# Optimization experiments

Hardware: AMD Instinct MI355X
Metric: run time of the kernel (lower is better)

## Reference

```python
import jax, jax.numpy as jnp
import numpy as np

SIGMA = 5.0
KSIZE = 31  # int(6*sigma+1), odd
CHANNEL = 3

def build_gaussian_kernel(size, sigma):
    coords = jnp.arange(size, dtype=jnp.float32) - size // 2
    g = jnp.exp(-coords ** 2 / (2.0 * sigma ** 2))
    g = g / g.sum()
    k2d = g[:, None] * g[None, :]            # (k, k)
    # depthwise kernel: (O=C, I/g=1, k, k)
    return jnp.broadcast_to(k2d[None, None], (CHANNEL, 1, size, size))

def depthwise_blur(x, kernel):
    # x: (B, C, H, W); kernel: (C, 1, k, k); groups = C, SAME-style padding k//2
    pad = KSIZE // 2
    return jax.lax.conv_general_dilated(
        x, kernel,
        window_strides=(1, 1),
        padding=((pad, pad), (pad, pad)),
        dimension_numbers=("NCHW", "OIHW", "NCHW"),
        feature_group_count=CHANNEL,
    )

def setup_inputs() -> dict:
    key = jax.random.key(0)
    k1, k2 = jax.random.split(key)
    B, C, H, W = 16, 3, 512, 512
    background = jax.random.uniform(k1, (B, C, H, W), dtype=jnp.float32)
    insatance = jax.random.uniform(k2, (B, C, H, W), dtype=jnp.float32)
    gaussian_kernel = build_gaussian_kernel(KSIZE, SIGMA)
    return {"background": background, "insatance": insatance,
            "gaussian_kernel": gaussian_kernel}

def reference(background, insatance, gaussian_kernel):
    # retinex_decompose(background): only illumination1 is used downstream
    bg_log = jnp.log1p(background)
    illumination1 = depthwise_blur(bg_log, gaussian_kernel)
    # retinex_decompose(insatance): reflectance2 = log1p(ins) - blur(log1p(ins))
    ins_log = jnp.log1p(insatance)
    illumination2 = depthwise_blur(ins_log, gaussian_kernel)
    reflectance2 = ins_log - illumination2
    # adjust_illumination(reflectance2, illumination1)
    img_log = reflectance2 + illumination1
    img_corrected = jnp.clip(jnp.expm1(img_log), 0.0, 1.0)
    return img_corrected
```

## Files before the change

### kernel.cpp

```cpp
#include <hip/hip_runtime.h>


constexpr int W_ = 512, H_ = 512;
constexpr int NIMG = 48;
constexpr int TW = 64, TH = 64;
constexpr int R_ = TH + 30;
constexpr int CSLOT = 24;
constexpr int DSTRIDE = 25;
constexpr int HSTRIDE = 17;

__device__ constexpr float G[31] = {
    8.8805851e-04f, 1.5861066e-03f, 2.7217699e-03f, 4.4874399e-03f,
    7.1084368e-03f, 1.0818767e-02f, 1.5820117e-02f, 2.2226435e-02f,
    3.0002549e-02f, 3.8911209e-02f, 4.8486352e-02f, 5.8048702e-02f,
    6.6771901e-02f, 7.3794364e-02f, 7.8357552e-02f, 7.9940480e-02f,
    7.8357552e-02f, 7.3794364e-02f, 6.6771901e-02f, 5.8048702e-02f,
    4.8486352e-02f, 3.8911209e-02f, 3.0002549e-02f, 2.2226435e-02f,
    1.5820117e-02f, 1.0818767e-02f, 7.1084368e-03f, 4.4874399e-03f,
    2.7217699e-03f, 1.5861066e-03f, 8.8805851e-04f};

__global__ __launch_bounds__(256) void retinex_fused(const float* __restrict__ bg,
                                                     const float* __restrict__ ins,
                                                     float* __restrict__ out) {
  __shared__ float4 sd[R_ * DSTRIDE];
  __shared__ float4 sh[R_ * HSTRIDE];

  const int tid = threadIdx.x;
  const int x0 = blockIdx.x * TW;
  const int y0 = blockIdx.y * TH;
  const size_t base = (size_t)blockIdx.z * ((size_t)H_ * W_);

#pragma unroll
  for (int it = 0; it < 9; ++it) {
    const int idx = tid + 256 * it;
    if (idx < R_ * CSLOT) {
      const int r = idx / CSLOT;
      const int c = idx - r * CSLOT;
      const int y = y0 - 15 + r;
      const int gx = x0 - 16 + 4 * c;
      float4 v = make_float4(0.f, 0.f, 0.f, 0.f);
      if ((unsigned)y < (unsigned)H_ && (unsigned)gx < (unsigned)W_) {
        const size_t a = base + (size_t)y * W_ + gx;
        const float4 b = *(const float4*)(bg + a);
        const float4 n = *(const float4*)(ins + a);
        v.x = __logf(1.f + b.x) - __logf(1.f + n.x);
        v.y = __logf(1.f + b.y) - __logf(1.f + n.y);
        v.z = __logf(1.f + b.z) - __logf(1.f + n.z);
        v.w = __logf(1.f + b.w) - __logf(1.f + n.w);
      }
      sd[r * DSTRIDE + c] = v;
    }
  }
  __syncthreads();

#pragma unroll
  for (int it = 0; it < 3; ++it) {
    const int idx = tid + 256 * it;
    if (idx < R_ * 8) {
      const int r = idx >> 3;
      const int w = idx & 7;
      float win[40];
      const float4* p = &sd[r * DSTRIDE + 2 * w];
#pragma unroll
      for (int k = 0; k < 10; ++k) {
        const float4 v = p[k];
        win[4 * k + 0] = v.x; win[4 * k + 1] = v.y;
        win[4 * k + 2] = v.z; win[4 * k + 3] = v.w;
      }
      float o[8];
#pragma unroll
      for (int e = 0; e < 8; ++e) {
        float a = 0.f;
#pragma unroll
        for (int c = 0; c < 31; ++c) a += G[c] * win[e + 1 + c];
        o[e] = a;
      }
      sh[r * HSTRIDE + 2 * w]     = make_float4(o[0], o[1], o[2], o[3]);
      sh[r * HSTRIDE + 2 * w + 1] = make_float4(o[4], o[5], o[6], o[7]);
    }
  }
  __syncthreads();

  {
    const int col = tid & 63;
    const int g = tid >> 6;
    const float* hf = (const float*)sh;
    float acc[16];
#pragma unroll
    for (int p = 0; p < 16; ++p) acc[p] = 0.f;
#pragma unroll
    for (int j = 0; j < 46; ++j) {
      const float v = hf[(16 * g + j) * (HSTRIDE * 4) + col];
#pragma unroll
      for (int p = 0; p < 16; ++p) {
        const int c = j - p;
        if (c >= 0 && c < 31) acc[p] += G[c] * v;
      }
    }
#pragma unroll
    for (int p = 0; p < 16; ++p) {
      const int y = y0 + 16 * g + p;
      const size_t idx = base + (size_t)y * W_ + x0 + col;
      const float il = __logf(1.f + ins[idx]);
      float r = __expf(il + acc[p]) - 1.f;
      out[idx] = fminf(fmaxf(r, 0.f), 1.f);
    }
  }
}

extern "C" void kernel_launch(void* const* d_in, const int* in_sizes, int n_in,
                              void* d_out, int out_size, void* d_ws, size_t ws_size,
                              hipStream_t stream) {
  const float* bg  = (const float*)d_in[0];
  const float* ins = (const float*)d_in[1];
  float* out = (float*)d_out;
  retinex_fused<<<dim3(W_ / TW, H_ / TH, NIMG), dim3(256), 0, stream>>>(bg, ins, out);
}
```

Baseline: 188.8 us.

## Split blur into vertical and horizontal passes through a transposed workspace

Replaces the single fused kernel with two kernels. The first does the vertical blur on log-differences and writes a transposed intermediate. The second reads that transposed data, so its horizontal blur becomes a column-wise register sweep, then applies the expm1 and clip. This removes the shared-memory horizontal pass and its halo columns, at the cost of an extra global write and read of a full intermediate buffer plus a second launch. If the workspace is too small it writes into an input buffer, which is risky.

```diff
diff --git a/kernel.cpp b/kernel.cpp
--- a/kernel.cpp
+++ b/kernel.cpp
@@ -1,13 +1,10 @@
 #include <hip/hip_runtime.h>
 
 
-constexpr int W_ = 512, H_ = 512;
-constexpr int NIMG = 48;
-constexpr int TW = 64, TH = 64;
-constexpr int R_ = TH + 30;
-constexpr int CSLOT = 24;
-constexpr int DSTRIDE = 25;
-constexpr int HSTRIDE = 17;
+constexpr int W_ = 512, H_ = 512, NIMG = 48;
+constexpr int TS = 64;
+constexpr int RS = 94;
+constexpr int PITCH = 68;
 
 __device__ constexpr float G[31] = {
     8.8805851e-04f, 1.5861066e-03f, 2.7217699e-03f, 4.4874399e-03f,
@@ -19,28 +16,25 @@
     1.5820117e-02f, 1.0818767e-02f, 7.1084368e-03f, 4.4874399e-03f,
     2.7217699e-03f, 1.5861066e-03f, 8.8805851e-04f};
 
-__global__ __launch_bounds__(256) void retinex_fused(const float* __restrict__ bg,
-                                                     const float* __restrict__ ins,
-                                                     float* __restrict__ out) {
-  __shared__ float4 sd[R_ * DSTRIDE];
-  __shared__ float4 sh[R_ * HSTRIDE];
-
-  const int tid = threadIdx.x;
-  const int x0 = blockIdx.x * TW;
-  const int y0 = blockIdx.y * TH;
+__global__ __launch_bounds__(256) void vpass(const float* __restrict__ bg,
+                                             const float* __restrict__ ins,
+                                             float* __restrict__ tmpT) {
+  __shared__ __align__(16) float sb[RS * PITCH];
+  const int tid  = threadIdx.x;
+  const int lane = tid & 63;
+  const int w    = tid >> 6;
+  const int x0 = blockIdx.x * TS, y0 = blockIdx.y * TS;
   const size_t base = (size_t)blockIdx.z * ((size_t)H_ * W_);
 
 #pragma unroll
-  for (int it = 0; it < 9; ++it) {
+  for (int it = 0; it < 6; ++it) {
     const int idx = tid + 256 * it;
-    if (idx < R_ * CSLOT) {
-      const int r = idx / CSLOT;
-      const int c = idx - r * CSLOT;
+    if (idx < RS * 16) {
+      const int r = idx >> 4, c = idx & 15;
       const int y = y0 - 15 + r;
-      const int gx = x0 - 16 + 4 * c;
       float4 v = make_float4(0.f, 0.f, 0.f, 0.f);
-      if ((unsigned)y < (unsigned)H_ && (unsigned)gx < (unsigned)W_) {
-        const size_t a = base + (size_t)y * W_ + gx;
+      if ((unsigned)y < (unsigned)H_) {
+        const size_t a = base + (size_t)y * W_ + x0 + 4 * c;
         const float4 b = *(const float4*)(bg + a);
         const float4 n = *(const float4*)(ins + a);
         v.x = __logf(1.f + b.x) - __logf(1.f + n.x);
@@ -48,63 +42,97 @@
         v.z = __logf(1.f + b.z) - __logf(1.f + n.z);
         v.w = __logf(1.f + b.w) - __logf(1.f + n.w);
       }
-      sd[r * DSTRIDE + c] = v;
+      *(float4*)(sb + r * PITCH + 4 * c) = v;
     }
   }
   __syncthreads();
 
+  float acc[16];
 #pragma unroll
-  for (int it = 0; it < 3; ++it) {
-    const int idx = tid + 256 * it;
-    if (idx < R_ * 8) {
-      const int r = idx >> 3;
-      const int w = idx & 7;
-      float win[40];
-      const float4* p = &sd[r * DSTRIDE + 2 * w];
+  for (int p = 0; p < 16; ++p) acc[p] = 0.f;
 #pragma unroll
-      for (int k = 0; k < 10; ++k) {
-        const float4 v = p[k];
-        win[4 * k + 0] = v.x; win[4 * k + 1] = v.y;
-        win[4 * k + 2] = v.z; win[4 * k + 3] = v.w;
-      }
-      float o[8];
+  for (int j = 0; j < 46; ++j) {
+    const float v = sb[(16 * w + j) * PITCH + lane];
 #pragma unroll
-      for (int e = 0; e < 8; ++e) {
-        float a = 0.f;
-#pragma unroll
-        for (int c = 0; c < 31; ++c) a += G[c] * win[e + 1 + c];
-        o[e] = a;
-      }
-      sh[r * HSTRIDE + 2 * w]     = make_float4(o[0], o[1], o[2], o[3]);
-      sh[r * HSTRIDE + 2 * w + 1] = make_float4(o[4], o[5], o[6], o[7]);
+    for (int p = 0; p < 16; ++p) {
+      const int c = j - p;
+      if (c >= 0 && c < 31) acc[p] += G[c] * v;
     }
   }
   __syncthreads();
 
-  {
-    const int col = tid & 63;
-    const int g = tid >> 6;
-    const float* hf = (const float*)sh;
-    float acc[16];
+  float4* st4 = (float4*)sb;
 #pragma unroll
-    for (int p = 0; p < 16; ++p) acc[p] = 0.f;
+  for (int q = 0; q < 4; ++q)
+    st4[lane * 17 + 4 * w + q] =
+        make_float4(acc[4 * q], acc[4 * q + 1], acc[4 * q + 2], acc[4 * q + 3]);
+  __syncthreads();
 #pragma unroll
-    for (int j = 0; j < 46; ++j) {
-      const float v = hf[(16 * g + j) * (HSTRIDE * 4) + col];
+  for (int it = 0; it < 4; ++it) {
+    const int idx = tid + 256 * it;
+    const int x = idx >> 4, y4 = idx & 15;
+    const float4 v = st4[x * 17 + y4];
+    *(float4*)(tmpT + base + (size_t)(x0 + x) * H_ + y0 + 4 * y4) = v;
+  }
+}
+
+__global__ __launch_bounds__(256) void hpass(const float* __restrict__ tmpT,
+                                             const float* __restrict__ ins,
+                                             float* __restrict__ out) {
+  __shared__ __align__(16) float sb[RS * PITCH];
+  const int tid  = threadIdx.x;
+  const int lane = tid & 63;
+  const int w    = tid >> 6;
+  const int x0 = blockIdx.x * TS, y0 = blockIdx.y * TS;
+  const size_t base = (size_t)blockIdx.z * ((size_t)H_ * W_);
+
 #pragma unroll
-      for (int p = 0; p < 16; ++p) {
-        const int c = j - p;
-        if (c >= 0 && c < 31) acc[p] += G[c] * v;
-      }
+  for (int it = 0; it < 6; ++it) {
+    const int idx = tid + 256 * it;
+    if (idx < RS * 16) {
+      const int r = idx >> 4, c = idx & 15;
+      const int x = x0 - 15 + r;
+      float4 v = make_float4(0.f, 0.f, 0.f, 0.f);
+      if ((unsigned)x < (unsigned)W_)
+        v = *(const float4*)(tmpT + base + (size_t)x * H_ + y0 + 4 * c);
+      *(float4*)(sb + r * PITCH + 4 * c) = v;
     }
+  }
+  __syncthreads();
+
+  float acc[16];
+#pragma unroll
+  for (int p = 0; p < 16; ++p) acc[p] = 0.f;
+#pragma unroll
+  for (int j = 0; j < 46; ++j) {
+    const float v = sb[(16 * w + j) * PITCH + lane];
 #pragma unroll
     for (int p = 0; p < 16; ++p) {
-      const int y = y0 + 16 * g + p;
-      const size_t idx = base + (size_t)y * W_ + x0 + col;
-      const float il = __logf(1.f + ins[idx]);
-      float r = __expf(il + acc[p]) - 1.f;
-      out[idx] = fminf(fmaxf(r, 0.f), 1.f);
+      const int c = j - p;
+      if (c >= 0 && c < 31) acc[p] += G[c] * v;
     }
+  }
+  __syncthreads();
+
+  float4* st4 = (float4*)sb;
+#pragma unroll
+  for (int q = 0; q < 4; ++q)
+    st4[lane * 17 + 4 * w + q] =
+        make_float4(acc[4 * q], acc[4 * q + 1], acc[4 * q + 2], acc[4 * q + 3]);
+  __syncthreads();
+#pragma unroll
+  for (int it = 0; it < 4; ++it) {
+    const int idx = tid + 256 * it;
+    const int y = idx >> 4, x4 = idx & 15;
+    const float4 b = st4[y * 17 + x4];
+    const size_t a = base + (size_t)(y0 + y) * W_ + x0 + 4 * x4;
+    const float4 n = *(const float4*)(ins + a);
+    float4 o;
+    o.x = fminf(fmaxf(__expf(__logf(1.f + n.x) + b.x) - 1.f, 0.f), 1.f);
+    o.y = fminf(fmaxf(__expf(__logf(1.f + n.y) + b.y) - 1.f, 0.f), 1.f);
+    o.z = fminf(fmaxf(__expf(__logf(1.f + n.z) + b.z) - 1.f, 0.f), 1.f);
+    o.w = fminf(fmaxf(__expf(__logf(1.f + n.w) + b.w) - 1.f, 0.f), 1.f);
+    *(float4*)(out + a) = o;
   }
 }
 
@@ -114,5 +142,11 @@
   const float* bg  = (const float*)d_in[0];
   const float* ins = (const float*)d_in[1];
   float* out = (float*)d_out;
-  retinex_fused<<<dim3(W_ / TW, H_ / TH, NIMG), dim3(256), 0, stream>>>(bg, ins, out);
+
+  const size_t need = (size_t)NIMG * H_ * W_ * sizeof(float);
+  float* tmpT = (ws_size >= need) ? (float*)d_ws : (float*)d_in[0];
+
+  dim3 grid(W_ / TS, H_ / TS, NIMG);
+  vpass<<<grid, dim3(256), 0, stream>>>(bg, ins, tmpT);
+  hpass<<<grid, dim3(256), 0, stream>>>(tmpT, ins, out);
 }
```

Result: faster. 171.8 us (-9.0%).

## Roll tile vertically with ring buffer and register prefetch of next strip

Applied to the files above, without the earlier changes.

Each block now covers a 64x256 column strip processed in 32-row steps. Horizontally blurred rows are kept in a 64-row ring buffer in shared memory, so the vertical halo is no longer recomputed for every 64x64 tile. Global loads for the next strip are prefetched into registers while the current strip is processed. The cost is fewer blocks (768 instead of 3072), more barriers per block, and an occupancy hint of 3 blocks per CU that may limit parallelism.

```diff
diff --git a/kernel.cpp b/kernel.cpp
--- a/kernel.cpp
+++ b/kernel.cpp
@@ -1,13 +1,9 @@
 #include <hip/hip_runtime.h>
 
 
-constexpr int W_ = 512, H_ = 512;
-constexpr int NIMG = 48;
-constexpr int TW = 64, TH = 64;
-constexpr int R_ = TH + 30;
-constexpr int CSLOT = 24;
-constexpr int DSTRIDE = 25;
-constexpr int HSTRIDE = 17;
+constexpr int W_ = 512, H_ = 512, NIMG = 48;
+constexpr int SPITCH = 100;
+constexpr int RPITCH = 68;
 
 __device__ constexpr float G[31] = {
     8.8805851e-04f, 1.5861066e-03f, 2.7217699e-03f, 4.4874399e-03f,
@@ -19,53 +15,78 @@
     1.5820117e-02f, 1.0818767e-02f, 7.1084368e-03f, 4.4874399e-03f,
     2.7217699e-03f, 1.5861066e-03f, 8.8805851e-04f};
 
-__global__ __launch_bounds__(256) void retinex_fused(const float* __restrict__ bg,
-                                                     const float* __restrict__ ins,
-                                                     float* __restrict__ out) {
-  __shared__ float4 sd[R_ * DSTRIDE];
-  __shared__ float4 sh[R_ * HSTRIDE];
+__global__ __launch_bounds__(256, 3) void retinex_roll(const float* __restrict__ bg,
+                                                       const float* __restrict__ ins,
+                                                       float* __restrict__ out) {
+  __shared__ __align__(16) float sd[32 * SPITCH];
+  __shared__ __align__(16) float hr[64 * RPITCH];
 
-  const int tid = threadIdx.x;
-  const int x0 = blockIdx.x * TW;
-  const int y0 = blockIdx.y * TH;
-  const size_t base = (size_t)blockIdx.z * ((size_t)H_ * W_);
+  const int tid  = threadIdx.x;
+  const int lane = tid & 63;
+  const int x0 = blockIdx.x * 64;
+  const int y0 = blockIdx.y * 256;
+  const size_t base = (size_t)blockIdx.z * (size_t)(H_ * W_);
 
+  int sr[3], sc[3], gx[3]; bool okx[3];
 #pragma unroll
-  for (int it = 0; it < 9; ++it) {
-    const int idx = tid + 256 * it;
-    if (idx < R_ * CSLOT) {
-      const int r = idx / CSLOT;
-      const int c = idx - r * CSLOT;
-      const int y = y0 - 15 + r;
-      const int gx = x0 - 16 + 4 * c;
-      float4 v = make_float4(0.f, 0.f, 0.f, 0.f);
-      if ((unsigned)y < (unsigned)H_ && (unsigned)gx < (unsigned)W_) {
-        const size_t a = base + (size_t)y * W_ + gx;
-        const float4 b = *(const float4*)(bg + a);
-        const float4 n = *(const float4*)(ins + a);
-        v.x = __logf(1.f + b.x) - __logf(1.f + n.x);
-        v.y = __logf(1.f + b.y) - __logf(1.f + n.y);
-        v.z = __logf(1.f + b.z) - __logf(1.f + n.z);
-        v.w = __logf(1.f + b.w) - __logf(1.f + n.w);
-      }
-      sd[r * DSTRIDE + c] = v;
+  for (int s = 0; s < 3; ++s) {
+    const int item = tid + 256 * s;
+    sr[s] = item / 24;
+    sc[s] = item - 24 * sr[s];
+    gx[s] = x0 - 16 + 4 * sc[s];
+    okx[s] = (unsigned)gx[s] < (unsigned)W_;
+  }
+  const int hrow = tid >> 3;
+  const int hcg  = tid & 7;
+  const int eg   = tid >> 6;
+
+  float4 pb[3], pn[3];
+#pragma unroll
+  for (int s = 0; s < 3; ++s) {
+    const int gy = y0 - 15 + sr[s];
+    pb[s] = make_float4(0.f, 0.f, 0.f, 0.f);
+    pn[s] = pb[s];
+    if (okx[s] && (unsigned)gy < (unsigned)H_) {
+      const size_t a = base + (size_t)gy * W_ + gx[s];
+      pb[s] = *(const float4*)(bg + a);
+      pn[s] = *(const float4*)(ins + a);
     }
   }
-  __syncthreads();
 
+#pragma unroll 1
+  for (int k = 0; k < 9; ++k) {
 #pragma unroll
-  for (int it = 0; it < 3; ++it) {
-    const int idx = tid + 256 * it;
-    if (idx < R_ * 8) {
-      const int r = idx >> 3;
-      const int w = idx & 7;
+    for (int s = 0; s < 3; ++s) {
+      float4 v;
+      v.x = __logf(1.f + pb[s].x) - __logf(1.f + pn[s].x);
+      v.y = __logf(1.f + pb[s].y) - __logf(1.f + pn[s].y);
+      v.z = __logf(1.f + pb[s].z) - __logf(1.f + pn[s].z);
+      v.w = __logf(1.f + pb[s].w) - __logf(1.f + pn[s].w);
+      *(float4*)(sd + sr[s] * SPITCH + 4 * sc[s]) = v;
+    }
+    if (k < 8) {
+#pragma unroll
+      for (int s = 0; s < 3; ++s) {
+        const int gy = y0 + 32 * (k + 1) - 15 + sr[s];
+        float4 b0 = make_float4(0.f, 0.f, 0.f, 0.f), n0 = b0;
+        if (okx[s] && (unsigned)gy < (unsigned)H_) {
+          const size_t a = base + (size_t)gy * W_ + gx[s];
+          b0 = *(const float4*)(bg + a);
+          n0 = *(const float4*)(ins + a);
+        }
+        pb[s] = b0; pn[s] = n0;
+      }
+    }
+    __syncthreads();
+
+    {
       float win[40];
-      const float4* p = &sd[r * DSTRIDE + 2 * w];
+      const float4* p4 = (const float4*)(sd + hrow * SPITCH) + 2 * hcg;
 #pragma unroll
-      for (int k = 0; k < 10; ++k) {
-        const float4 v = p[k];
-        win[4 * k + 0] = v.x; win[4 * k + 1] = v.y;
-        win[4 * k + 2] = v.z; win[4 * k + 3] = v.w;
+      for (int q = 0; q < 10; ++q) {
+        const float4 v = p4[q];
+        win[4 * q + 0] = v.x; win[4 * q + 1] = v.y;
+        win[4 * q + 2] = v.z; win[4 * q + 3] = v.w;
       }
       float o[8];
 #pragma unroll
@@ -75,35 +96,35 @@
         for (int c = 0; c < 31; ++c) a += G[c] * win[e + 1 + c];
         o[e] = a;
       }
-      sh[r * HSTRIDE + 2 * w]     = make_float4(o[0], o[1], o[2], o[3]);
-      sh[r * HSTRIDE + 2 * w + 1] = make_float4(o[4], o[5], o[6], o[7]);
+      const int slot = (32 * k - 15 + hrow + 128) & 63;
+      float* dst = hr + slot * RPITCH + 8 * hcg;
+      *(float4*)(dst)     = make_float4(o[0], o[1], o[2], o[3]);
+      *(float4*)(dst + 4) = make_float4(o[4], o[5], o[6], o[7]);
     }
-  }
-  __syncthreads();
+    __syncthreads();
 
-  {
-    const int col = tid & 63;
-    const int g = tid >> 6;
-    const float* hf = (const float*)sh;
-    float acc[16];
+    if (k >= 1) {
+      const int t0 = 32 * (k - 1) + 8 * eg;
+      float acc[8];
 #pragma unroll
-    for (int p = 0; p < 16; ++p) acc[p] = 0.f;
+      for (int p = 0; p < 8; ++p) acc[p] = 0.f;
 #pragma unroll
-    for (int j = 0; j < 46; ++j) {
-      const float v = hf[(16 * g + j) * (HSTRIDE * 4) + col];
+      for (int j = 0; j < 38; ++j) {
+        const int lr = t0 - 15 + j;
+        const float v = hr[((lr + 128) & 63) * RPITCH + lane];
 #pragma unroll
-      for (int p = 0; p < 16; ++p) {
-        const int c = j - p;
-        if (c >= 0 && c < 31) acc[p] += G[c] * v;
+        for (int p = 0; p < 8; ++p) {
+          const int c = j - p;
+          if (c >= 0 && c < 31) acc[p] += G[c] * v;
+        }
       }
-    }
 #pragma unroll
-    for (int p = 0; p < 16; ++p) {
-      const int y = y0 + 16 * g + p;
-      const size_t idx = base + (size_t)y * W_ + x0 + col;
-      const float il = __logf(1.f + ins[idx]);
-      float r = __expf(il + acc[p]) - 1.f;
-      out[idx] = fminf(fmaxf(r, 0.f), 1.f);
+      for (int p = 0; p < 8; ++p) {
+        const size_t a = base + (size_t)(y0 + t0 + p) * W_ + x0 + lane;
+        const float il = __logf(1.f + ins[a]);
+        float r = __expf(il + acc[p]) - 1.f;
+        out[a] = fminf(fmaxf(r, 0.f), 1.f);
+      }
     }
   }
 }
@@ -114,5 +135,5 @@
   const float* bg  = (const float*)d_in[0];
   const float* ins = (const float*)d_in[1];
   float* out = (float*)d_out;
-  retinex_fused<<<dim3(W_ / TW, H_ / TH, NIMG), dim3(256), 0, stream>>>(bg, ins, out);
+  retinex_roll<<<dim3(8, 2, NIMG), dim3(256), 0, stream>>>(bg, ins, out);
 }
```

Measured after the change: 161.9 us. 14.2% less time.
